# Kernel optimization log

Measured on AMD Instinct MI355X. Metric: run time of the kernel, lower is better.

Reference implementation:

```python
import jax, jax.numpy as jnp
import numpy as np

B, T, S, D = 8, 2048, 2048, 256


def setup_inputs() -> dict:
    key = jax.random.key(0)
    k1, k2, k3, k4 = jax.random.split(key, 4)
    source = jax.random.normal(k1, (B, T, D), dtype=jnp.float32)
    memory_bank = jax.random.normal(k2, (B, S, D), dtype=jnp.float32)
    # torch Linear(2*dim, dim, bias=False); stored as [in, out] so y = x @ W_out
    W_out = jax.random.normal(k3, (2 * D, D), dtype=jnp.float32) * 0.05
    memory_lengths = jax.random.randint(k4, (B,), 1, S + 1, dtype=jnp.int64)
    return {"source": source, "memory_bank": memory_bank, "W_out": W_out,
            "memory_lengths": memory_lengths}


def reference(source, memory_bank, W_out, memory_lengths):
    # align[b,t,s] = <source[b,t], memory_bank[b,s]>   (attn_type='dot')
    align = jnp.einsum('btd,bsd->bts', source, memory_bank)
    # sequence mask over source positions
    mask = jnp.arange(S)[None, :] < memory_lengths[:, None]          # [B,S]
    align = jnp.where(mask[:, None, :], align, -jnp.inf)             # [B,T,S]
    # coverage branch (multi-step): exp of shifted scores
    maxes = jnp.max(align, axis=2, keepdims=True)
    exp_score = jnp.exp(align - maxes)                               # [B,T,S]
    # tril-ones bmm == shifted cumulative sum over target steps:
    # penalty[t] = sum_{j<t} exp_score[j] for t>=1, penalty[0] = 1
    penalty = jnp.cumsum(exp_score[:, :-1, :], axis=1)
    penalty = jnp.concatenate(
        [jnp.ones_like(exp_score[:, :1, :]), penalty], axis=1)
    unnormalized = exp_score / (penalty + 1e-20)
    align_vectors = unnormalized / jnp.sum(unnormalized, axis=2, keepdims=True)
    # context and output projection
    c = jnp.einsum('bts,bsd->btd', align_vectors, memory_bank)
    concat_c = jnp.concatenate([c, source], axis=-1)                 # [B,T,2D]
    attn_h = jnp.tanh(concat_c @ W_out)                              # [B,T,D]
    return attn_h, align_vectors
```

## Files before the change

### kernel.cpp

```cpp
#include <hip/hip_runtime.h>
#include <math.h>

#define BN 8
#define TT 2048
#define SS 2048
#define DD 256
#define NSEG 128
#define SEGLEN 16

typedef __attribute__((ext_vector_type(8))) short short8;
typedef __attribute__((ext_vector_type(4))) float floatx4;

__device__ __forceinline__ unsigned short f2bf_rne(float f) {
    unsigned int u = __float_as_uint(f);
    u = (u + 0x7FFFu + ((u >> 16) & 1u)) >> 16;
    return (unsigned short)u;
}
__device__ __forceinline__ float bf2f(unsigned short h) {
    return __uint_as_float(((unsigned int)h) << 16);
}
__device__ __forceinline__ unsigned int fenc(float f) {
    unsigned int b = __float_as_uint(f);
    return (b & 0x80000000u) ? ~b : (b | 0x80000000u);
}
__device__ __forceinline__ float fdec(unsigned int u) {
    return __uint_as_float((u & 0x80000000u) ? (u & 0x7FFFFFFFu) : ~u);
}

__device__ __forceinline__ void async16(const unsigned short* g, unsigned short* l) {
    __builtin_amdgcn_global_load_lds(
        (const __attribute__((address_space(1))) unsigned int*)g,
        (__attribute__((address_space(3))) unsigned int*)l,
        16, 0, 0);
}

__global__ __launch_bounds__(256) void kpre(
    const float* __restrict__ src, const float* __restrict__ mem,
    unsigned short* __restrict__ shi, unsigned short* __restrict__ slo,
    unsigned short* __restrict__ mhirm, unsigned short* __restrict__ mlorm,
    unsigned int* __restrict__ rowmaxU)
{
    if (blockIdx.y == 0 && blockIdx.x < (BN * TT / 256))
        rowmaxU[blockIdx.x * 256 + threadIdx.x] = 0u;
    const float* in; unsigned short *oh, *ol;
    if (blockIdx.y == 0) { in = src; oh = shi; ol = slo; }
    else                 { in = mem; oh = mhirm; ol = mlorm; }
    const size_t base = ((size_t)blockIdx.x * 256 + threadIdx.x) * 8;
    float4 v0 = *(const float4*)(in + base);
    float4 v1 = *(const float4*)(in + base + 4);
    float f[8] = {v0.x, v0.y, v0.z, v0.w, v1.x, v1.y, v1.z, v1.w};
    short8 hv, lv;
#pragma unroll
    for (int j = 0; j < 8; j++) {
        unsigned short h = f2bf_rne(f[j]);
        hv[j] = (short)h;
        lv[j] = (short)f2bf_rne(f[j] - bf2f(h));
    }
    *(short8*)(oh + base) = hv;
    *(short8*)(ol + base) = lv;
}

__global__ __launch_bounds__(256) void k1_mfma(
    const unsigned short* __restrict__ shi, const unsigned short* __restrict__ slo,
    const unsigned short* __restrict__ mhirm, const unsigned short* __restrict__ mlorm,
    const int* __restrict__ lens, float* __restrict__ alignb,
    unsigned int* __restrict__ rowmaxU)
{
    const int b  = blockIdx.z;
    const int len = lens[b];
    const int s0 = blockIdx.x * 128;
    if (s0 >= len) return;
    const int t0 = blockIdx.y * 128;
    const int tid = threadIdx.x;
    const int wave = tid >> 6, lane = tid & 63;
    const int wt = wave & 1, wsb = wave >> 1;
    const int quad = lane >> 4, m = lane & 15;

    __shared__ unsigned short ldsAh[128 * 32];
    __shared__ unsigned short ldsAl[128 * 32];
    __shared__ unsigned short ldsBh[128 * 32];
    __shared__ unsigned short ldsBl[128 * 32];

    const int srow = tid >> 2, sk4 = (tid & 3) * 8;
    const size_t aBase = ((size_t)(b * TT + t0 + srow)) * DD + sk4;
    const size_t bBase = ((size_t)(b * SS + s0 + srow)) * DD + sk4;
    const size_t aBase2 = aBase + (size_t)64 * DD;
    const size_t bBase2 = bBase + (size_t)64 * DD;
    const int lo1 = tid * 8, lo2 = tid * 8 + 2048;

    floatx4 acc[4][4];
#pragma unroll
    for (int i = 0; i < 4; i++)
#pragma unroll
        for (int j = 0; j < 4; j++) acc[i][j] = (floatx4)0.f;

    for (int kc = 0; kc < 8; kc++) {
        const int ko = kc * 32;
        __syncthreads();
        async16(shi   + aBase  + ko, ldsAh + lo1);
        async16(shi   + aBase2 + ko, ldsAh + lo2);
        async16(slo   + aBase  + ko, ldsAl + lo1);
        async16(slo   + aBase2 + ko, ldsAl + lo2);
        async16(mhirm + bBase  + ko, ldsBh + lo1);
        async16(mhirm + bBase2 + ko, ldsBh + lo2);
        async16(mlorm + bBase  + ko, ldsBl + lo1);
        async16(mlorm + bBase2 + ko, ldsBl + lo2);
        __syncthreads();

        short8 Ah[4], Al[4], Bh[4], Bl[4];
#pragma unroll
        for (int f = 0; f < 4; f++) {
            const int ra = (wt * 64 + f * 16 + m) * 32 + quad * 8;
            const int rb = (wsb * 64 + f * 16 + m) * 32 + quad * 8;
            Ah[f] = *(const short8*)&ldsAh[ra];
            Al[f] = *(const short8*)&ldsAl[ra];
            Bh[f] = *(const short8*)&ldsBh[rb];
            Bl[f] = *(const short8*)&ldsBl[rb];
        }
#pragma unroll
        for (int mf = 0; mf < 4; mf++)
#pragma unroll
            for (int nf = 0; nf < 4; nf++) {
                acc[mf][nf] = __builtin_amdgcn_mfma_f32_16x16x32_bf16(
                    Ah[mf], Bh[nf], acc[mf][nf], 0, 0, 0);
                acc[mf][nf] = __builtin_amdgcn_mfma_f32_16x16x32_bf16(
                    Al[mf], Bh[nf], acc[mf][nf], 0, 0, 0);
                acc[mf][nf] = __builtin_amdgcn_mfma_f32_16x16x32_bf16(
                    Ah[mf], Bl[nf], acc[mf][nf], 0, 0, 0);
            }
    }

#pragma unroll
    for (int mf = 0; mf < 4; mf++)
#pragma unroll
        for (int reg = 0; reg < 4; reg++) {
            const int t = t0 + wt * 64 + mf * 16 + quad * 4 + reg;
            float* row = alignb + ((size_t)(b * TT + t)) * SS + s0 + wsb * 64 + m;
#pragma unroll
            for (int nf = 0; nf < 4; nf++)
                row[nf * 16] = acc[mf][nf][reg];
        }

    if (s0 + wsb * 64 < len) {
#pragma unroll
        for (int mf = 0; mf < 4; mf++)
#pragma unroll
            for (int reg = 0; reg < 4; reg++) {
                float mx = -INFINITY;
#pragma unroll
                for (int nf = 0; nf < 4; nf++) {
                    const int col = s0 + wsb * 64 + nf * 16 + m;
                    mx = (col < len) ? fmaxf(mx, acc[mf][nf][reg]) : mx;
                }
#pragma unroll
                for (int off = 1; off < 16; off <<= 1)
                    mx = fmaxf(mx, __shfl_xor(mx, off, 64));
                if (m == 0) {
                    const int t = t0 + wt * 64 + mf * 16 + quad * 4 + reg;
                    atomicMax(&rowmaxU[b * TT + t], fenc(mx));
                }
            }
    }
}

__global__ __launch_bounds__(256) void k3_segsum(
    const float* __restrict__ alignb, const unsigned int* __restrict__ rowmaxU,
    const int* __restrict__ lens, float* __restrict__ segsum)
{
    const int b = blockIdx.z, seg = blockIdx.y;
    const int s = blockIdx.x * 256 + threadIdx.x;
    const size_t oidx = ((size_t)b * NSEG + seg) * SS + s;
    if (s >= lens[b]) { segsum[oidx] = 0.f; return; }
    const float* base = alignb + ((size_t)b * TT + seg * SEGLEN) * SS + s;
    const unsigned int* rmu = rowmaxU + b * TT + seg * SEGLEN;
    float sum = 0.f;
#pragma unroll 4
    for (int r = 0; r < SEGLEN; r++)
        sum += __expf(base[(size_t)r * SS] - fdec(rmu[r]));
    segsum[oidx] = sum;
}

__global__ __launch_bounds__(256) void k4_prefix(float* __restrict__ segsum)
{
    const int b = blockIdx.y;
    const int s = blockIdx.x * 256 + threadIdx.x;
    float run = 0.f;
    for (int g = 0; g < NSEG / 8; g++) {
        float v[8];
#pragma unroll
        for (int i = 0; i < 8; i++)
            v[i] = segsum[((size_t)b * NSEG + g * 8 + i) * SS + s];
#pragma unroll
        for (int i = 0; i < 8; i++) {
            segsum[((size_t)b * NSEG + g * 8 + i) * SS + s] = run;
            run += v[i];
        }
    }
}

__global__ __launch_bounds__(256) void k6pre(
    const float* __restrict__ mem, unsigned short* __restrict__ mhi)
{
    const int gid = blockIdx.x * 256 + threadIdx.x;
    const int lane = gid & 63;
    const int dt   = (gid >> 6) & 15;
    const int c    = (gid >> 10) & 63;
    const int b    = gid >> 16;
    const int quad = lane >> 4, n = lane & 15;
    const int s = c * 32 + quad * 8;
    const int d = dt * 16 + n;
    const float* srcp = mem + ((size_t)b * SS + s) * DD + d;
    short8 hi;
#pragma unroll
    for (int j = 0; j < 8; j++)
        hi[j] = (short)f2bf_rne(srcp[(size_t)j * DD]);
    *(short8*)(mhi + (size_t)gid * 8) = hi;
}

__global__ __launch_bounds__(256) void k5_scan(
    float* __restrict__ alignb, const unsigned int* __restrict__ rowmaxU,
    const float* __restrict__ segsum, const int* __restrict__ lens)
{
    const int seg = blockIdx.x, b = blockIdx.y;
    const int len = lens[b];
    const int c0 = threadIdx.x * 8;
    const int lane = threadIdx.x & 63, wid = threadIdx.x >> 6;
    const bool anyv = c0 < len;

    __shared__ float red[8];

    float psum[8];
    {
        const float* sp = segsum + ((size_t)b * NSEG + seg) * SS + c0;
        float4 a = *(const float4*)sp, c = *(const float4*)(sp + 4);
        psum[0] = a.x; psum[1] = a.y; psum[2] = a.z; psum[3] = a.w;
        psum[4] = c.x; psum[5] = c.y; psum[6] = c.z; psum[7] = c.w;
    }

    float* rowp = alignb + ((size_t)(b * TT + seg * SEGLEN)) * SS + c0;

    float avn[8] = {0.f, 0.f, 0.f, 0.f, 0.f, 0.f, 0.f, 0.f};
    if (anyv) {
        float4 a = *(const float4*)rowp, c = *(const float4*)(rowp + 4);
        avn[0] = a.x; avn[1] = a.y; avn[2] = a.z; avn[3] = a.w;
        avn[4] = c.x; avn[5] = c.y; avn[6] = c.z; avn[7] = c.w;
    }

    for (int r = 0; r < SEGLEN; r++) {
        const int t = seg * SEGLEN + r;
        const float m = fdec(rowmaxU[b * TT + t]);
        float av[8];
#pragma unroll
        for (int j = 0; j < 8; j++) av[j] = avn[j];
        if (anyv && r + 1 < SEGLEN) {
            const float* np = rowp + (size_t)(r + 1) * SS;
            float4 a = *(const float4*)np, c = *(const float4*)(np + 4);
            avn[0] = a.x; avn[1] = a.y; avn[2] = a.z; avn[3] = a.w;
            avn[4] = c.x; avn[5] = c.y; avn[6] = c.z; avn[7] = c.w;
        }
        float u[8], rsum = 0.f;
#pragma unroll
        for (int j = 0; j < 8; j++) {
            float e = (c0 + j < len) ? __expf(av[j] - m) : 0.f;
            float div = (t == 0) ? 1.0f : (psum[j] + 1e-20f);
            u[j] = e * __builtin_amdgcn_rcpf(div);
            psum[j] += e;
            rsum += u[j];
        }
#pragma unroll
        for (int off = 32; off > 0; off >>= 1)
            rsum += __shfl_down(rsum, off, 64);
        const int pp = (r & 1) * 4;
        if (lane == 0) red[pp + wid] = rsum;
        __syncthreads();
        const float inv = 1.0f / (red[pp] + red[pp + 1] + red[pp + 2] + red[pp + 3]);
        float* wp = rowp + (size_t)r * SS;
        float4 o0 = {u[0] * inv, u[1] * inv, u[2] * inv, u[3] * inv};
        float4 o1 = {u[4] * inv, u[5] * inv, u[6] * inv, u[7] * inv};
        *(float4*)wp = o0;
        *(float4*)(wp + 4) = o1;
    }
}

__global__ __launch_bounds__(256, 4) void k6_context(
    const float* __restrict__ alignb, const unsigned short* __restrict__ mhi,
    const int* __restrict__ lens, float* __restrict__ cfull)
{
    const int b  = blockIdx.x;
    const int t0 = blockIdx.y * 32;
    const int tid  = threadIdx.x;
    const int wave = tid >> 6, lane = tid & 63;
    const int quad = lane >> 4, m = lane & 15;

    const int len = lens[b];
    int cmax = (len + 31) >> 5;
    if (cmax > 64) cmax = 64;

    floatx4 acc[2][4];
#pragma unroll
    for (int i = 0; i < 2; i++)
#pragma unroll
        for (int j = 0; j < 4; j++) acc[i][j] = (floatx4)0.f;

    const float* aBase = alignb + ((size_t)(b * TT + t0 + m)) * SS + quad * 8;

    for (int c = 0; c < cmax; c++) {
        short8 Bf[4];
#pragma unroll
        for (int j = 0; j < 4; j++) {
            const int dt = wave * 4 + j;
            Bf[j] = *(const short8*)(mhi +
                (((size_t)(b * 64 + c) * 16 + dt) * 64 + lane) * 8);
        }
#pragma unroll
        for (int mf = 0; mf < 2; mf++) {
            const float* ap = aBase + (size_t)(mf * 16) * SS + c * 32;
            float4 v0 = *(const float4*)ap;
            float4 v1 = *(const float4*)(ap + 4);
            union { short8 s; unsigned int u[4]; } pk;
            pk.u[0] = (__float_as_uint(v0.x) >> 16) | (__float_as_uint(v0.y) & 0xFFFF0000u);
            pk.u[1] = (__float_as_uint(v0.z) >> 16) | (__float_as_uint(v0.w) & 0xFFFF0000u);
            pk.u[2] = (__float_as_uint(v1.x) >> 16) | (__float_as_uint(v1.y) & 0xFFFF0000u);
            pk.u[3] = (__float_as_uint(v1.z) >> 16) | (__float_as_uint(v1.w) & 0xFFFF0000u);
#pragma unroll
            for (int j = 0; j < 4; j++)
                acc[mf][j] = __builtin_amdgcn_mfma_f32_16x16x32_bf16(
                    pk.s, Bf[j], acc[mf][j], 0, 0, 0);
        }
    }

#pragma unroll
    for (int mf = 0; mf < 2; mf++)
#pragma unroll
        for (int j = 0; j < 4; j++) {
            const int d = wave * 64 + j * 16 + m;
#pragma unroll
            for (int reg = 0; reg < 4; reg++) {
                const int t = t0 + mf * 16 + quad * 4 + reg;
                cfull[((size_t)(b * TT + t)) * DD + d] = acc[mf][j][reg];
            }
        }
}

__global__ __launch_bounds__(256) void k7_out(
    const float* __restrict__ cfull, const float* __restrict__ src,
    const float* __restrict__ W, float* __restrict__ attn)
{
    const int b = blockIdx.y;
    const int t0 = blockIdx.x * 32;
    const int tid = threadIdx.x;
    const int tx = tid & 63, ty = tid >> 6;

    __shared__ __align__(16) float wT[32][256];
    __shared__ float xT[32][32];

    float4 acc[8];
#pragma unroll
    for (int i = 0; i < 8; i++) acc[i] = make_float4(0.f, 0.f, 0.f, 0.f);

    for (int k0 = 0; k0 < 2 * DD; k0 += 32) {
        __syncthreads();
#pragma unroll
        for (int it = 0; it < 8; it++) {
            int f = tid + it * 256;
            int kr = f >> 6, col = (f & 63) * 4;
            *(float4*)&wT[kr][col] =
                *(const float4*)(W + (size_t)(k0 + kr) * DD + col);
        }
#pragma unroll
        for (int rep = 0; rep < 4; rep++) {
            int idx = tid + rep * 256;
            int r = idx >> 5, c = idx & 31;
            int k = k0 + c;
            float x;
            if (k < DD) {
                x = cfull[((size_t)b * TT + t0 + r) * DD + k];
            } else {
                x = src[((size_t)b * TT + t0 + r) * DD + (k - DD)];
            }
            xT[r][c] = x;
        }
        __syncthreads();
#pragma unroll
        for (int kk = 0; kk < 32; kk++) {
            float4 w4 = *(const float4*)&wT[kk][tx * 4];
#pragma unroll
            for (int r4 = 0; r4 < 8; r4++) {
                float x = xT[ty + r4 * 4][kk];
                acc[r4].x += x * w4.x; acc[r4].y += x * w4.y;
                acc[r4].z += x * w4.z; acc[r4].w += x * w4.w;
            }
        }
    }
#pragma unroll
    for (int r4 = 0; r4 < 8; r4++) {
        const int t = t0 + ty + r4 * 4;
        float4 o;
        o.x = tanhf(acc[r4].x); o.y = tanhf(acc[r4].y);
        o.z = tanhf(acc[r4].z); o.w = tanhf(acc[r4].w);
        *(float4*)(attn + ((size_t)b * TT + t) * DD + tx * 4) = o;
    }
}

extern "C" void kernel_launch(void* const* d_in, const int* in_sizes, int n_in,
                              void* d_out, int out_size, void* d_ws, size_t ws_size,
                              hipStream_t stream)
{
    const float* src  = (const float*)d_in[0];
    const float* mem  = (const float*)d_in[1];
    const float* Wout = (const float*)d_in[2];
    const int*   lens = (const int*)d_in[3];

    float* out    = (float*)d_out;
    float* attn   = out;
    float* alignb = out + (size_t)BN * TT * DD;

    unsigned int* rowmaxU = (unsigned int*)d_ws;
    float* segsum = (float*)(rowmaxU + (size_t)BN * TT);
    unsigned short* mhi = (unsigned short*)(segsum + (size_t)BN * NSEG * SS);
    unsigned short* shi   = mhi + (size_t)BN * SS * DD;
    unsigned short* slo   = shi + (size_t)BN * TT * DD;
    unsigned short* mhirm = slo + (size_t)BN * TT * DD;
    unsigned short* mlorm = mhirm + (size_t)BN * SS * DD;
    float* cfull = (float*)shi;

    kpre<<<dim3(BN * TT * DD / (256 * 8), 2), 256, 0, stream>>>(
        src, mem, shi, slo, mhirm, mlorm, rowmaxU);
    k6pre<<<dim3(BN * 64 * 16 * 64 / 256), 256, 0, stream>>>(mem, mhi);
    k1_mfma<<<dim3(SS / 128, TT / 128, BN), 256, 0, stream>>>(
        shi, slo, mhirm, mlorm, lens, alignb, rowmaxU);
    k3_segsum<<<dim3(SS / 256, NSEG, BN), 256, 0, stream>>>(alignb, rowmaxU, lens, segsum);
    k4_prefix<<<dim3(SS / 256, BN), 256, 0, stream>>>(segsum);
    k5_scan<<<dim3(NSEG, BN), 256, 0, stream>>>(alignb, rowmaxU, segsum, lens);
    k6_context<<<dim3(BN, TT / 32), 256, 0, stream>>>(alignb, mhi, lens, cfull);
    k7_out<<<dim3(TT / 32, BN), 256, 0, stream>>>(cfull, src, Wout, attn);
}
```

Measured before the change: 425.4 us.

## Fuse context and output projection, merge prep kernels, vectorize segsum

Result: slower. 437.6 us (+2.9%).

```diff
diff --git a/kernel.cpp b/kernel.cpp
--- a/kernel.cpp
+++ b/kernel.cpp
@@ -34,12 +34,29 @@
         16, 0, 0);
 }
 
-__global__ __launch_bounds__(256) void kpre(
+__global__ __launch_bounds__(256) void kprep(
     const float* __restrict__ src, const float* __restrict__ mem,
     unsigned short* __restrict__ shi, unsigned short* __restrict__ slo,
     unsigned short* __restrict__ mhirm, unsigned short* __restrict__ mlorm,
-    unsigned int* __restrict__ rowmaxU)
-{
+    unsigned short* __restrict__ mhi, unsigned int* __restrict__ rowmaxU)
+{
+    if (blockIdx.y == 2) {
+        const int gid = blockIdx.x * 256 + threadIdx.x;
+        const int lane = gid & 63;
+        const int dt   = (gid >> 6) & 15;
+        const int c    = (gid >> 10) & 63;
+        const int b    = gid >> 16;
+        const int quad = lane >> 4, n = lane & 15;
+        const int s = c * 32 + quad * 8;
+        const int d = dt * 16 + n;
+        const float* srcp = mem + ((size_t)b * SS + s) * DD + d;
+        short8 hi;
+#pragma unroll
+        for (int j = 0; j < 8; j++)
+            hi[j] = (short)f2bf_rne(srcp[(size_t)j * DD]);
+        *(short8*)(mhi + (size_t)gid * 8) = hi;
+        return;
+    }
     if (blockIdx.y == 0 && blockIdx.x < (BN * TT / 256))
         rowmaxU[blockIdx.x * 256 + threadIdx.x] = 0u;
     const float* in; unsigned short *oh, *ol;
@@ -168,16 +185,24 @@
     const int* __restrict__ lens, float* __restrict__ segsum)
 {
     const int b = blockIdx.z, seg = blockIdx.y;
-    const int s = blockIdx.x * 256 + threadIdx.x;
-    const size_t oidx = ((size_t)b * NSEG + seg) * SS + s;
-    if (s >= lens[b]) { segsum[oidx] = 0.f; return; }
-    const float* base = alignb + ((size_t)b * TT + seg * SEGLEN) * SS + s;
-    const unsigned int* rmu = rowmaxU + b * TT + seg * SEGLEN;
-    float sum = 0.f;
+    const int s4 = (blockIdx.x * 256 + threadIdx.x) * 4;
+    const int len = lens[b];
+    float4 sum = {0.f, 0.f, 0.f, 0.f};
+    if (s4 < len) {
+        const float* base = alignb + ((size_t)b * TT + seg * SEGLEN) * SS + s4;
+        const unsigned int* rmu = rowmaxU + b * TT + seg * SEGLEN;
+        const bool v1 = (s4 + 1) < len, v2 = (s4 + 2) < len, v3 = (s4 + 3) < len;
 #pragma unroll 4
-    for (int r = 0; r < SEGLEN; r++)
-        sum += __expf(base[(size_t)r * SS] - fdec(rmu[r]));
-    segsum[oidx] = sum;
+        for (int r = 0; r < SEGLEN; r++) {
+            const float m = fdec(rmu[r]);
+            float4 v = *(const float4*)(base + (size_t)r * SS);
+            sum.x += __expf(v.x - m);
+            sum.y += v1 ? __expf(v.y - m) : 0.f;
+            sum.z += v2 ? __expf(v.z - m) : 0.f;
+            sum.w += v3 ? __expf(v.w - m) : 0.f;
+        }
+    }
+    *(float4*)(segsum + ((size_t)b * NSEG + seg) * SS + s4) = sum;
 }
 
 __global__ __launch_bounds__(256) void k4_prefix(float* __restrict__ segsum)
@@ -196,25 +221,6 @@
             run += v[i];
         }
     }
-}
-
-__global__ __launch_bounds__(256) void k6pre(
-    const float* __restrict__ mem, unsigned short* __restrict__ mhi)
-{
-    const int gid = blockIdx.x * 256 + threadIdx.x;
-    const int lane = gid & 63;
-    const int dt   = (gid >> 6) & 15;
-    const int c    = (gid >> 10) & 63;
-    const int b    = gid >> 16;
-    const int quad = lane >> 4, n = lane & 15;
-    const int s = c * 32 + quad * 8;
-    const int d = dt * 16 + n;
-    const float* srcp = mem + ((size_t)b * SS + s) * DD + d;
-    short8 hi;
-#pragma unroll
-    for (int j = 0; j < 8; j++)
-        hi[j] = (short)f2bf_rne(srcp[(size_t)j * DD]);
-    *(short8*)(mhi + (size_t)gid * 8) = hi;
 }
 
 __global__ __launch_bounds__(256) void k5_scan(
@@ -282,15 +288,20 @@
     }
 }
 
-__global__ __launch_bounds__(256, 4) void k6_context(
+__global__ __launch_bounds__(256) void k67_ctx_out(
     const float* __restrict__ alignb, const unsigned short* __restrict__ mhi,
-    const int* __restrict__ lens, float* __restrict__ cfull)
+    const int* __restrict__ lens, const float* __restrict__ src,
+    const float* __restrict__ W, float* __restrict__ attn)
 {
     const int b  = blockIdx.x;
     const int t0 = blockIdx.y * 32;
     const int tid  = threadIdx.x;
     const int wave = tid >> 6, lane = tid & 63;
     const int quad = lane >> 4, m = lane & 15;
+
+    __shared__ __align__(16) float cT[32][256];
+    __shared__ __align__(16) float wT[32][256];
+    __shared__ float xT[32][32];
 
     const int len = lens[b];
     int cmax = (len + 31) >> 5;
@@ -335,28 +346,15 @@
         for (int j = 0; j < 4; j++) {
             const int d = wave * 64 + j * 16 + m;
 #pragma unroll
-            for (int reg = 0; reg < 4; reg++) {
-                const int t = t0 + mf * 16 + quad * 4 + reg;
-                cfull[((size_t)(b * TT + t)) * DD + d] = acc[mf][j][reg];
-            }
-        }
-}
-
-__global__ __launch_bounds__(256) void k7_out(
-    const float* __restrict__ cfull, const float* __restrict__ src,
-    const float* __restrict__ W, float* __restrict__ attn)
-{
-    const int b = blockIdx.y;
-    const int t0 = blockIdx.x * 32;
-    const int tid = threadIdx.x;
+            for (int reg = 0; reg < 4; reg++)
+                cT[mf * 16 + quad * 4 + reg][d] = acc[mf][j][reg];
+        }
+
     const int tx = tid & 63, ty = tid >> 6;
 
-    __shared__ __align__(16) float wT[32][256];
-    __shared__ float xT[32][32];
-
-    float4 acc[8];
-#pragma unroll
-    for (int i = 0; i < 8; i++) acc[i] = make_float4(0.f, 0.f, 0.f, 0.f);
+    float4 oacc[8];
+#pragma unroll
+    for (int i = 0; i < 8; i++) oacc[i] = make_float4(0.f, 0.f, 0.f, 0.f);
 
     for (int k0 = 0; k0 < 2 * DD; k0 += 32) {
         __syncthreads();
@@ -374,7 +372,7 @@
             int k = k0 + c;
             float x;
             if (k < DD) {
-                x = cfull[((size_t)b * TT + t0 + r) * DD + k];
+                x = cT[r][k];
             } else {
                 x = src[((size_t)b * TT + t0 + r) * DD + (k - DD)];
             }
@@ -387,8 +385,8 @@
 #pragma unroll
             for (int r4 = 0; r4 < 8; r4++) {
                 float x = xT[ty + r4 * 4][kk];
-                acc[r4].x += x * w4.x; acc[r4].y += x * w4.y;
-                acc[r4].z += x * w4.z; acc[r4].w += x * w4.w;
+                oacc[r4].x += x * w4.x; oacc[r4].y += x * w4.y;
+                oacc[r4].z += x * w4.z; oacc[r4].w += x * w4.w;
             }
         }
     }
@@ -396,8 +394,8 @@
     for (int r4 = 0; r4 < 8; r4++) {
         const int t = t0 + ty + r4 * 4;
         float4 o;
-        o.x = tanhf(acc[r4].x); o.y = tanhf(acc[r4].y);
-        o.z = tanhf(acc[r4].z); o.w = tanhf(acc[r4].w);
+        o.x = tanhf(oacc[r4].x); o.y = tanhf(oacc[r4].y);
+        o.z = tanhf(oacc[r4].z); o.w = tanhf(oacc[r4].w);
         *(float4*)(attn + ((size_t)b * TT + t) * DD + tx * 4) = o;
     }
 }
@@ -422,16 +420,14 @@
     unsigned short* slo   = shi + (size_t)BN * TT * DD;
     unsigned short* mhirm = slo + (size_t)BN * TT * DD;
     unsigned short* mlorm = mhirm + (size_t)BN * SS * DD;
-    float* cfull = (float*)shi;
-
-    kpre<<<dim3(BN * TT * DD / (256 * 8), 2), 256, 0, stream>>>(
-        src, mem, shi, slo, mhirm, mlorm, rowmaxU);
-    k6pre<<<dim3(BN * 64 * 16 * 64 / 256), 256, 0, stream>>>(mem, mhi);
+
+    kprep<<<dim3(BN * TT * DD / (256 * 8), 3), 256, 0, stream>>>(
+        src, mem, shi, slo, mhirm, mlorm, mhi, rowmaxU);
     k1_mfma<<<dim3(SS / 128, TT / 128, BN), 256, 0, stream>>>(
         shi, slo, mhirm, mlorm, lens, alignb, rowmaxU);
-    k3_segsum<<<dim3(SS / 256, NSEG, BN), 256, 0, stream>>>(alignb, rowmaxU, lens, segsum);
+    k3_segsum<<<dim3(SS / 1024, NSEG, BN), 256, 0, stream>>>(alignb, rowmaxU, lens, segsum);
     k4_prefix<<<dim3(SS / 256, BN), 256, 0, stream>>>(segsum);
     k5_scan<<<dim3(NSEG, BN), 256, 0, stream>>>(alignb, rowmaxU, segsum, lens);
-    k6_context<<<dim3(BN, TT / 32), 256, 0, stream>>>(alignb, mhi, lens, cfull);
-    k7_out<<<dim3(TT / 32, BN), 256, 0, stream>>>(cfull, src, Wout, attn);
-}
+    k67_ctx_out<<<dim3(BN, TT / 32), 256, 0, stream>>>(
+        alignb, mhi, lens, src, Wout, attn);
+}
```
